# Kernel optimization log

Hardware: AMD Instinct MI355X
Metric: run time of the kernel (lower is better)

Reference implementation:

```python
import jax, jax.numpy as jnp
import numpy as np

B, S, H = 1, 4096, 768
NH, HD = 12, 64
THETA = 160000.0
WINDOW = 64  # local_attention=128 // 2
NEG = -1e9


def _rope_tables(seq_len, dim, theta):
    inv_freq = 1.0 / (theta ** (np.arange(0, dim, 2, dtype=np.float32) / dim))  # [dim/2]
    t = np.arange(seq_len, dtype=np.float32)
    freqs = np.outer(t, inv_freq)                      # [S, dim/2]
    emb = np.concatenate([freqs, freqs], axis=-1)      # [S, dim]
    return jnp.asarray(np.cos(emb)), jnp.asarray(np.sin(emb))


def _sliding_causal_mask(seq_len, window):
    i = np.arange(seq_len)[:, None]
    j = np.arange(seq_len)[None, :]
    allowed = (j <= i) & (i - j <= window)
    mask = np.where(allowed, 0.0, NEG).astype(np.float32)
    return jnp.asarray(mask)[None, None]  # [1,1,S,S]


def rotate_half(x):
    d = x.shape[-1] // 2
    return jnp.concatenate([-x[..., d:], x[..., :d]], axis=-1)


def setup_inputs() -> dict:
    key = jax.random.key(0)
    k1, k2, k3 = jax.random.split(key, 3)
    hidden_states = jax.random.normal(k1, (B, S, H), dtype=jnp.float32)
    w_qkv = jax.random.normal(k2, (3 * H, H), dtype=jnp.float32) * (H ** -0.5)
    w_o = jax.random.normal(k3, (H, H), dtype=jnp.float32) * (H ** -0.5)
    cos, sin = _rope_tables(S, HD, THETA)
    attention_mask = _sliding_causal_mask(S, WINDOW)
    return {"hidden_states": hidden_states, "w_qkv": w_qkv, "w_o": w_o,
            "cos": cos, "sin": sin, "attention_mask": attention_mask}


def reference(hidden_states, w_qkv, w_o, cos, sin, attention_mask):
    b, s, h = hidden_states.shape
    # QKV projection (no bias; attention_bias=False)
    qkv = jnp.einsum('bsh,oh->bso', hidden_states, w_qkv)        # [B,S,3H]
    qkv = qkv.reshape(b, s, 3, NH, HD)
    q = jnp.transpose(qkv[:, :, 0], (0, 2, 1, 3))                # [B,NH,S,HD]
    k = jnp.transpose(qkv[:, :, 1], (0, 2, 1, 3))
    v = jnp.transpose(qkv[:, :, 2], (0, 2, 1, 3))
    # RoPE
    c = cos[None, None]; sn = sin[None, None]                    # [1,1,S,HD]
    q = q * c + rotate_half(q) * sn
    k = k * c + rotate_half(k) * sn
    # eager attention: scaled QK^T + additive causal/sliding mask, fp32 softmax
    scaling = HD ** -0.5
    scores = jnp.einsum('bhqd,bhkd->bhqk', q, k) * scaling
    scores = scores + attention_mask[:, :, :, :s]
    attn = jax.nn.softmax(scores.astype(jnp.float32), axis=-1).astype(q.dtype)
    out = jnp.einsum('bhqk,bhkd->bhqd', attn, v)                 # [B,NH,S,HD]
    out = jnp.transpose(out, (0, 2, 1, 3)).reshape(b, s, h)
    return jnp.einsum('bsh,oh->bso', out, w_o)                   # Wo projection
```

## Files before the change

kernel.cpp:

```cpp
#include <hip/hip_runtime.h>

#define SLEN   4096
#define HDIM   768
#define NHEADS 12
#define HEADD  64
#define NQKV   2304
#define WIN    64

constexpr float SCALE = 0.125f;
constexpr float LOG2E = 1.4426950408889634f;

typedef short bf16x8 __attribute__((ext_vector_type(8)));
typedef float f32x4  __attribute__((ext_vector_type(4)));
typedef unsigned short u16;

#define MFMA(a, b, c) __builtin_amdgcn_mfma_f32_16x16x32_bf16((a), (b), (c), 0, 0, 0)

#define GLDS(gp, lp) __builtin_amdgcn_global_load_lds( \
    (const __attribute__((address_space(1))) unsigned*)(gp), \
    (__attribute__((address_space(3))) unsigned*)(lp), 16, 0, 0)

__device__ inline u16 f2bf(float x) {
    unsigned u = __float_as_uint(x);
    u += 0x7fff + ((u >> 16) & 1);
    return (u16)(u >> 16);
}
__device__ inline float bf2f(u16 b) { return __uint_as_float(((unsigned)b) << 16); }
__device__ inline unsigned packsplit(float x) {
    u16 h = f2bf(x);
    u16 l = f2bf(x - bf2f(h));
    return (unsigned)h | ((unsigned)l << 16);
}

__global__ __launch_bounds__(256) void split_planes(
    const float* __restrict__ hs, const float* __restrict__ wq, const float* __restrict__ wo,
    u16* __restrict__ hsH, u16* __restrict__ hsL,
    u16* __restrict__ wqH, u16* __restrict__ wqL,
    u16* __restrict__ woH, u16* __restrict__ woL)
{
    int qid = blockIdx.x * 256 + threadIdx.x;
    const float* src; u16 *dH, *dL; int r, k8;
    if (qid < 393216)      { src = hs; dH = hsH; dL = hsL; r = qid / 96; k8 = qid % 96; }
    else if (qid < 614400) { int q = qid - 393216; src = wq; dH = wqH; dL = wqL; r = q / 96; k8 = q % 96; }
    else                   { int q = qid - 614400; src = wo; dH = woH; dL = woL; r = q / 96; k8 = q % 96; }

    const float* p = src + (size_t)r * 768 + k8 * 8;
    float4 f0 = *(const float4*)p, f1 = *(const float4*)(p + 4);
    float fv[8] = {f0.x, f0.y, f0.z, f0.w, f1.x, f1.y, f1.z, f1.w};
    unsigned hh[4], ll[4];
#pragma unroll
    for (int i = 0; i < 4; ++i) {
        u16 h0 = f2bf(fv[2*i]),   h1 = f2bf(fv[2*i+1]);
        u16 l0 = f2bf(fv[2*i] - bf2f(h0)), l1 = f2bf(fv[2*i+1] - bf2f(h1));
        hh[i] = (unsigned)h0 | ((unsigned)h1 << 16);
        ll[i] = (unsigned)l0 | ((unsigned)l1 << 16);
    }
    size_t di = (size_t)r * 768 + (k8 >> 2) * 32 + (size_t)(((k8 & 3) ^ (r & 3))) * 8;
    *(uint4*)(dH + di) = uint4{hh[0], hh[1], hh[2], hh[3]};
    *(uint4*)(dL + di) = uint4{ll[0], ll[1], ll[2], ll[3]};
}

template <int MODE>
__global__ __launch_bounds__(256) void gemm_sp(
    const u16* __restrict__ Ah, const u16* __restrict__ Al,
    const u16* __restrict__ Bh, const u16* __restrict__ Bl,
    void* __restrict__ Cv, int M, int N, int K,
    const float* __restrict__ cosT, const float* __restrict__ sinT)
{
    __shared__ u16 sAh[4096], sAl[4096], sBh[4096], sBl[4096];

    const int tid = threadIdx.x;
    const int w = tid >> 6, lane = tid & 63;
    const int wr = w >> 1, wc = w & 1;
    const int l15 = lane & 15, l4 = lane >> 4;
    const int rowBase = blockIdx.y * 128, colBase = blockIdx.x * 128;
    const size_t strB = (size_t)K * 2;

    const char* Ahb = (const char*)Ah; const char* Alb = (const char*)Al;
    const char* Bhb = (const char*)Bh; const char* Blb = (const char*)Bl;

    f32x4 acc[4][4];
#pragma unroll
    for (int m = 0; m < 4; ++m)
#pragma unroll
        for (int n = 0; n < 4; ++n) acc[m][n] = f32x4{0.f, 0.f, 0.f, 0.f};

    const int nkt = K >> 5;
    for (int kt = 0; kt < nkt; ++kt) {
#pragma unroll
        for (int i = 0; i < 2; ++i) {
            int row  = i * 64 + w * 16 + (lane >> 2);
            int quad = lane & 3;
            size_t goA = (size_t)(rowBase + row) * strB + kt * 64 + quad * 16;
            size_t goB = (size_t)(colBase + row) * strB + kt * 64 + quad * 16;
            unsigned lo = i * 4096 + w * 1024;
            GLDS(Ahb + goA, (char*)sAh + lo);
            GLDS(Alb + goA, (char*)sAl + lo);
            GLDS(Bhb + goB, (char*)sBh + lo);
            GLDS(Blb + goB, (char*)sBl + lo);
        }
        __syncthreads();

        bf16x8 ah[4], al[4];
#pragma unroll
        for (int m = 0; m < 4; ++m) {
            int row = wr * 64 + m * 16 + l15;
            int byt = row * 64 + ((l4 * 16) ^ ((row & 3) << 4));
            ah[m] = *(const bf16x8*)((const char*)sAh + byt);
            al[m] = *(const bf16x8*)((const char*)sAl + byt);
        }
#pragma unroll
        for (int n = 0; n < 4; ++n) {
            int row = wc * 64 + n * 16 + l15;
            int byt = row * 64 + ((l4 * 16) ^ ((row & 3) << 4));
            bf16x8 bh = *(const bf16x8*)((const char*)sBh + byt);
            bf16x8 bl = *(const bf16x8*)((const char*)sBl + byt);
#pragma unroll
            for (int m = 0; m < 4; ++m) {
                acc[m][n] = MFMA(ah[m], bh, acc[m][n]);
                acc[m][n] = MFMA(ah[m], bl, acc[m][n]);
                acc[m][n] = MFMA(al[m], bh, acc[m][n]);
            }
        }
        __syncthreads();
    }

    if constexpr (MODE == 0) {
        float* C = (float*)Cv;
#pragma unroll
        for (int m = 0; m < 4; ++m)
#pragma unroll
            for (int n = 0; n < 4; ++n)
#pragma unroll
                for (int j = 0; j < 4; ++j) {
                    int row = rowBase + wr * 64 + m * 16 + l4 * 4 + j;
                    int col = colBase + wc * 64 + n * 16 + l15;
                    C[(size_t)row * N + col] = acc[m][n][j];
                }
    } else {
        unsigned* QKVp = (unsigned*)Cv;
        const int span = colBase + wc * 64;
        const int t = span / HDIM;
        const int hh = (span - t * HDIM) >> 6;
        unsigned* dstH = QKVp + (((size_t)t * NHEADS + hh) * SLEN) * HEADD;
#pragma unroll
        for (int m = 0; m < 4; ++m)
#pragma unroll
            for (int np = 0; np < 2; ++np)
#pragma unroll
                for (int j = 0; j < 4; ++j) {
                    int srow = rowBase + wr * 64 + m * 16 + l4 * 4 + j;
                    int dlo = np * 16 + l15;
                    float lo = acc[m][np][j];
                    float hi = acc[m][np + 2][j];
                    unsigned* dst = dstH + (size_t)srow * HEADD;
                    if (t < 2) {
                        float c = cosT[srow * HEADD + dlo];
                        float s = sinT[srow * HEADD + dlo];
                        float nlo = lo * c - hi * s;
                        float nhi = hi * c + lo * s;
                        dst[dlo]      = packsplit(nlo);
                        dst[dlo + 32] = packsplit(nhi);
                    } else {
                        dst[dlo]      = packsplit(lo);
                        dst[dlo + 32] = packsplit(hi);
                    }
                }
    }
}

__global__ __launch_bounds__(256) void attn_mfma(
    const unsigned* __restrict__ QKV, u16* __restrict__ OAh, u16* __restrict__ OAl)
{
    const int h  = blockIdx.x >> 6;
    const int qt = blockIdx.x & 63;
    const int qbase = qt << 6;
    const int kwin = qbase - 64;

    __shared__ u16 VTh[64 * 128], VTl[64 * 128];
    __shared__ u16 Ph_s[4][16 * 72], Pl_s[4][16 * 72];

    const unsigned* Qg = QKV + ((size_t)(0 * NHEADS + h) * SLEN) * HEADD;
    const unsigned* Kg = QKV + ((size_t)(1 * NHEADS + h) * SLEN) * HEADD;
    const unsigned* Vg = QKV + ((size_t)(2 * NHEADS + h) * SLEN) * HEADD;

    const int tid = threadIdx.x;
    const int w = tid >> 6, lane = tid & 63;
    const int l15 = lane & 15, l4 = lane >> 4;

#pragma unroll
    for (int i = 0; i < 4; ++i) {
        int idx = i * 256 + tid;
        int key = idx >> 3;
        int d8  = (idx & 7) * 8;
        int kg = kwin + key; if (kg < 0) kg = 0;
        const unsigned* vp = Vg + (size_t)kg * 64 + d8;
        uint4 p0 = *(const uint4*)vp, p1 = *(const uint4*)(vp + 4);
        unsigned vv[8] = {p0.x, p0.y, p0.z, p0.w, p1.x, p1.y, p1.z, p1.w};
#pragma unroll
        for (int j = 0; j < 8; ++j) {
            int d = d8 + j;
            int kk = key ^ ((d & 15) << 3);
            VTh[d * 128 + kk] = (u16)(vv[j] & 0xffff);
            VTl[d * 128 + kk] = (u16)(vv[j] >> 16);
        }
    }
    __syncthreads();

    const int qrow = qbase + w * 16 + l15;
    bf16x8 qh[2], ql[2];
#pragma unroll
    for (int ks = 0; ks < 2; ++ks) {
        const unsigned* qp = Qg + (size_t)qrow * 64 + ks * 32 + l4 * 8;
        uint4 a = *(const uint4*)qp, b = *(const uint4*)(qp + 4);
        union { unsigned u[4]; bf16x8 v; } H, L;
        H.u[0] = __builtin_amdgcn_perm(a.y, a.x, 0x05040100);
        H.u[1] = __builtin_amdgcn_perm(a.w, a.z, 0x05040100);
        H.u[2] = __builtin_amdgcn_perm(b.y, b.x, 0x05040100);
        H.u[3] = __builtin_amdgcn_perm(b.w, b.z, 0x05040100);
        L.u[0] = __builtin_amdgcn_perm(a.y, a.x, 0x07060302);
        L.u[1] = __builtin_amdgcn_perm(a.w, a.z, 0x07060302);
        L.u[2] = __builtin_amdgcn_perm(b.y, b.x, 0x07060302);
        L.u[3] = __builtin_amdgcn_perm(b.w, b.z, 0x07060302);
        qh[ks] = H.v; ql[ks] = L.v;
    }

    f32x4 st[8];
#pragma unroll
    for (int t = 0; t < 8; ++t) st[t] = f32x4{0.f, 0.f, 0.f, 0.f};
#pragma unroll
    for (int t = 0; t < 8; ++t) {
        int krow = kwin + 16 * t + l15; if (krow < 0) krow = 0;
#pragma unroll
        for (int ks = 0; ks < 2; ++ks) {
            const unsigned* kp = Kg + (size_t)krow * 64 + ks * 32 + l4 * 8;
            uint4 a = *(const uint4*)kp, b = *(const uint4*)(kp + 4);
            union { unsigned u[4]; bf16x8 v; } H, L;
            H.u[0] = __builtin_amdgcn_perm(a.y, a.x, 0x05040100);
            H.u[1] = __builtin_amdgcn_perm(a.w, a.z, 0x05040100);
            H.u[2] = __builtin_amdgcn_perm(b.y, b.x, 0x05040100);
            H.u[3] = __builtin_amdgcn_perm(b.w, b.z, 0x05040100);
            L.u[0] = __builtin_amdgcn_perm(a.y, a.x, 0x07060302);
            L.u[1] = __builtin_amdgcn_perm(a.w, a.z, 0x07060302);
            L.u[2] = __builtin_amdgcn_perm(b.y, b.x, 0x07060302);
            L.u[3] = __builtin_amdgcn_perm(b.w, b.z, 0x07060302);
            st[t] = MFMA(H.v, qh[ks], st[t]);
            st[t] = MFMA(H.v, ql[ks], st[t]);
            st[t] = MFMA(L.v, qh[ks], st[t]);
        }
    }

    const int qg = qrow;
    float mx = -1e30f;
#pragma unroll
    for (int t = 0; t < 8; ++t)
#pragma unroll
        for (int j = 0; j < 4; ++j) {
            int kg = kwin + 16 * t + 4 * l4 + j;
            float s = st[t][j] * SCALE;
            bool ok = (kg >= 0) && (kg <= qg) && (qg - kg <= WIN);
            s = ok ? s : -1e30f;
            st[t][j] = s;
            mx = fmaxf(mx, s);
        }
    mx = fmaxf(mx, __shfl_xor(mx, 16));
    mx = fmaxf(mx, __shfl_xor(mx, 32));
    float lsum = 0.f;
#pragma unroll
    for (int t = 0; t < 8; ++t)
#pragma unroll
        for (int j = 0; j < 4; ++j) {
            float p = exp2f((st[t][j] - mx) * LOG2E);
            st[t][j] = p;
            lsum += p;
        }
    lsum += __shfl_xor(lsum, 16);
    lsum += __shfl_xor(lsum, 32);

    f32x4 o[4];
#pragma unroll
    for (int dt = 0; dt < 4; ++dt) o[dt] = f32x4{0.f, 0.f, 0.f, 0.f};

#pragma unroll
    for (int half = 0; half < 2; ++half) {
#pragma unroll
        for (int tt = 0; tt < 4; ++tt) {
            int t = half * 4 + tt;
            u16 phv[4], plv[4];
#pragma unroll
            for (int j = 0; j < 4; ++j) {
                float p = st[t][j];
                phv[j] = f2bf(p);
                plv[j] = f2bf(p - bf2f(phv[j]));
            }
            int pidx = l15 * 72 + tt * 16 + l4 * 4;
            *(uint2*)&Ph_s[w][pidx] = uint2{(unsigned)phv[0] | ((unsigned)phv[1] << 16),
                                            (unsigned)phv[2] | ((unsigned)phv[3] << 16)};
            *(uint2*)&Pl_s[w][pidx] = uint2{(unsigned)plv[0] | ((unsigned)plv[1] << 16),
                                            (unsigned)plv[2] | ((unsigned)plv[3] << 16)};
        }
#pragma unroll
        for (int kss = 0; kss < 2; ++kss) {
            int koff = kss * 32 + l4 * 8;
            bf16x8 pbh = *(const bf16x8*)&Ph_s[w][l15 * 72 + koff];
            bf16x8 pbl = *(const bf16x8*)&Pl_s[w][l15 * 72 + koff];
            int K0 = half * 64 + kss * 32 + l4 * 8;
            int kk = K0 ^ (l15 << 3);
#pragma unroll
            for (int dt = 0; dt < 4; ++dt) {
                int d = dt * 16 + l15;
                bf16x8 vh = *(const bf16x8*)&VTh[d * 128 + kk];
                bf16x8 vl = *(const bf16x8*)&VTl[d * 128 + kk];
                o[dt] = MFMA(vh, pbh, o[dt]);
                o[dt] = MFMA(vh, pbl, o[dt]);
                o[dt] = MFMA(vl, pbh, o[dt]);
            }
        }
    }

    float inv = 1.0f / lsum;
    const int srow = qrow;
#pragma unroll
    for (int dt = 0; dt < 4; ++dt) {
        u16 hv[4], lv[4];
#pragma unroll
        for (int j = 0; j < 4; ++j) {
            float v = o[dt][j] * inv;
            hv[j] = f2bf(v);
            lv[j] = f2bf(v - bf2f(hv[j]));
        }
        int col0 = h * 64 + dt * 16 + l4 * 4;
        size_t di = (size_t)srow * 768 + (col0 >> 5) * 32
                  + (size_t)((((col0 >> 3) & 3) ^ (srow & 3))) * 8 + (col0 & 7);
        *(uint2*)(OAh + di) = uint2{(unsigned)hv[0] | ((unsigned)hv[1] << 16),
                                    (unsigned)hv[2] | ((unsigned)hv[3] << 16)};
        *(uint2*)(OAl + di) = uint2{(unsigned)lv[0] | ((unsigned)lv[1] << 16),
                                    (unsigned)lv[2] | ((unsigned)lv[3] << 16)};
    }
}

extern "C" void kernel_launch(void* const* d_in, const int* in_sizes, int n_in,
                              void* d_out, int out_size, void* d_ws, size_t ws_size,
                              hipStream_t stream)
{
    const float* hs   = (const float*)d_in[0];
    const float* wqkv = (const float*)d_in[1];
    const float* wo   = (const float*)d_in[2];
    const float* cosT = (const float*)d_in[3];
    const float* sinT = (const float*)d_in[4];
    float* out = (float*)d_out;

    char* p = (char*)d_ws;
    unsigned* qkvP = (unsigned*)p;      p += (size_t)3 * NHEADS * SLEN * HEADD * 4;
    u16* hsH = (u16*)p;                 p += (size_t)SLEN * HDIM * 2;
    u16* hsL = (u16*)p;                 p += (size_t)SLEN * HDIM * 2;
    u16* wqH = (u16*)p;                 p += (size_t)NQKV * HDIM * 2;
    u16* wqL = (u16*)p;                 p += (size_t)NQKV * HDIM * 2;
    u16* woH = (u16*)p;                 p += (size_t)HDIM * HDIM * 2;
    u16* woL = (u16*)p;                 p += (size_t)HDIM * HDIM * 2;
    u16* oAh = hsH;
    u16* oAl = hsL;

    split_planes<<<2688, 256, 0, stream>>>(hs, wqkv, wo, hsH, hsL, wqH, wqL, woH, woL);

    dim3 g1(NQKV / 128, SLEN / 128);
    gemm_sp<1><<<g1, 256, 0, stream>>>(hsH, hsL, wqH, wqL, qkvP, SLEN, NQKV, HDIM, cosT, sinT);

    attn_mfma<<<NHEADS * (SLEN / 64), 256, 0, stream>>>(qkvP, oAh, oAl);

    dim3 g2(HDIM / 128, SLEN / 128);
    gemm_sp<0><<<g2, 256, 0, stream>>>(oAh, oAl, woH, woL, out, SLEN, HDIM, HDIM, nullptr, nullptr);
}
```

Before: 248.9 us.

## Double-buffer LDS in split-bf16 GEMM, swizzle block order, smaller M tile for Wo

The split-precision GEMM now double-buffers its LDS tiles, issuing the global-to-LDS loads for the next K step before computing the current one, and drops one barrier per iteration. Blocks are launched on a 1D grid and remapped in a stride-8 interleaved order, intended to spread neighbouring tiles across XCDs. The output projection uses a 64-row M tile so it launches 384 blocks instead of 192 and fills more CUs. The cost is doubled LDS use, which may lower occupancy, and the prefetch into the other buffer depends on the single barrier per iteration for correctness.

```diff
diff --git a/kernel.cpp b/kernel.cpp
--- a/kernel.cpp
+++ b/kernel.cpp
@@ -60,80 +60,98 @@
     *(uint4*)(dL + di) = uint4{ll[0], ll[1], ll[2], ll[3]};
 }
 
-template <int MODE>
+template <int BM, int MODE>
 __global__ __launch_bounds__(256) void gemm_sp(
     const u16* __restrict__ Ah, const u16* __restrict__ Al,
     const u16* __restrict__ Bh, const u16* __restrict__ Bl,
-    void* __restrict__ Cv, int M, int N, int K,
-    const float* __restrict__ cosT, const float* __restrict__ sinT)
+    void* __restrict__ Cv, int N, int K,
+    const float* __restrict__ cosT, const float* __restrict__ sinT, int NBX)
 {
-    __shared__ u16 sAh[4096], sAl[4096], sBh[4096], sBl[4096];
+    constexpr int ASZ = BM * 32;
+    constexpr int MF  = BM / 32;
+    __shared__ u16 sAh[2][ASZ], sAl[2][ASZ], sBh[2][4096], sBl[2][4096];
 
     const int tid = threadIdx.x;
     const int w = tid >> 6, lane = tid & 63;
     const int wr = w >> 1, wc = w & 1;
     const int l15 = lane & 15, l4 = lane >> 4;
-    const int rowBase = blockIdx.y * 128, colBase = blockIdx.x * 128;
+    const int quad = lane & 3, rl = lane >> 2;
+
+    const int cpx = gridDim.x >> 3;
+    const int bsw = (blockIdx.x & 7) * cpx + (blockIdx.x >> 3);
+    const int bx = bsw % NBX, by = bsw / NBX;
+    const int rowBase = by * BM, colBase = bx * 128;
+
     const size_t strB = (size_t)K * 2;
-
     const char* Ahb = (const char*)Ah; const char* Alb = (const char*)Al;
     const char* Bhb = (const char*)Bh; const char* Blb = (const char*)Bl;
 
-    f32x4 acc[4][4];
-#pragma unroll
-    for (int m = 0; m < 4; ++m)
+    f32x4 acc[MF][4];
+#pragma unroll
+    for (int m = 0; m < MF; ++m)
 #pragma unroll
         for (int n = 0; n < 4; ++n) acc[m][n] = f32x4{0.f, 0.f, 0.f, 0.f};
 
+    auto stage = [&](int bi, int kt) {
+        size_t kb = (size_t)kt * 64 + quad * 16;
+#pragma unroll
+        for (int i = 0; i < BM / 64; ++i) {
+            int row = i * 64 + w * 16 + rl;
+            size_t go = (size_t)(rowBase + row) * strB + kb;
+            unsigned lo = i * 4096 + w * 1024;
+            GLDS(Ahb + go, (char*)(&sAh[bi][0]) + lo);
+            GLDS(Alb + go, (char*)(&sAl[bi][0]) + lo);
+        }
+#pragma unroll
+        for (int i = 0; i < 2; ++i) {
+            int row = i * 64 + w * 16 + rl;
+            size_t go = (size_t)(colBase + row) * strB + kb;
+            unsigned lo = i * 4096 + w * 1024;
+            GLDS(Bhb + go, (char*)(&sBh[bi][0]) + lo);
+            GLDS(Blb + go, (char*)(&sBl[bi][0]) + lo);
+        }
+    };
+
     const int nkt = K >> 5;
+    stage(0, 0);
+    int cur = 0;
     for (int kt = 0; kt < nkt; ++kt) {
-#pragma unroll
-        for (int i = 0; i < 2; ++i) {
-            int row  = i * 64 + w * 16 + (lane >> 2);
-            int quad = lane & 3;
-            size_t goA = (size_t)(rowBase + row) * strB + kt * 64 + quad * 16;
-            size_t goB = (size_t)(colBase + row) * strB + kt * 64 + quad * 16;
-            unsigned lo = i * 4096 + w * 1024;
-            GLDS(Ahb + goA, (char*)sAh + lo);
-            GLDS(Alb + goA, (char*)sAl + lo);
-            GLDS(Bhb + goB, (char*)sBh + lo);
-            GLDS(Blb + goB, (char*)sBl + lo);
-        }
         __syncthreads();
-
-        bf16x8 ah[4], al[4];
-#pragma unroll
-        for (int m = 0; m < 4; ++m) {
-            int row = wr * 64 + m * 16 + l15;
+        if (kt + 1 < nkt) stage(cur ^ 1, kt + 1);
+
+        bf16x8 ah[MF], al[MF];
+#pragma unroll
+        for (int m = 0; m < MF; ++m) {
+            int row = wr * (MF * 16) + m * 16 + l15;
             int byt = row * 64 + ((l4 * 16) ^ ((row & 3) << 4));
-            ah[m] = *(const bf16x8*)((const char*)sAh + byt);
-            al[m] = *(const bf16x8*)((const char*)sAl + byt);
+            ah[m] = *(const bf16x8*)((const char*)(&sAh[cur][0]) + byt);
+            al[m] = *(const bf16x8*)((const char*)(&sAl[cur][0]) + byt);
         }
 #pragma unroll
         for (int n = 0; n < 4; ++n) {
             int row = wc * 64 + n * 16 + l15;
             int byt = row * 64 + ((l4 * 16) ^ ((row & 3) << 4));
-            bf16x8 bh = *(const bf16x8*)((const char*)sBh + byt);
-            bf16x8 bl = *(const bf16x8*)((const char*)sBl + byt);
-#pragma unroll
-            for (int m = 0; m < 4; ++m) {
+            bf16x8 bh = *(const bf16x8*)((const char*)(&sBh[cur][0]) + byt);
+            bf16x8 bl = *(const bf16x8*)((const char*)(&sBl[cur][0]) + byt);
+#pragma unroll
+            for (int m = 0; m < MF; ++m) {
                 acc[m][n] = MFMA(ah[m], bh, acc[m][n]);
                 acc[m][n] = MFMA(ah[m], bl, acc[m][n]);
                 acc[m][n] = MFMA(al[m], bh, acc[m][n]);
             }
         }
-        __syncthreads();
+        cur ^= 1;
     }
 
     if constexpr (MODE == 0) {
         float* C = (float*)Cv;
 #pragma unroll
-        for (int m = 0; m < 4; ++m)
+        for (int m = 0; m < MF; ++m)
 #pragma unroll
             for (int n = 0; n < 4; ++n)
 #pragma unroll
                 for (int j = 0; j < 4; ++j) {
-                    int row = rowBase + wr * 64 + m * 16 + l4 * 4 + j;
+                    int row = rowBase + wr * (MF * 16) + m * 16 + l4 * 4 + j;
                     int col = colBase + wc * 64 + n * 16 + l15;
                     C[(size_t)row * N + col] = acc[m][n][j];
                 }
@@ -144,12 +162,12 @@
         const int hh = (span - t * HDIM) >> 6;
         unsigned* dstH = QKVp + (((size_t)t * NHEADS + hh) * SLEN) * HEADD;
 #pragma unroll
-        for (int m = 0; m < 4; ++m)
+        for (int m = 0; m < MF; ++m)
 #pragma unroll
             for (int np = 0; np < 2; ++np)
 #pragma unroll
                 for (int j = 0; j < 4; ++j) {
-                    int srow = rowBase + wr * 64 + m * 16 + l4 * 4 + j;
+                    int srow = rowBase + wr * (MF * 16) + m * 16 + l4 * 4 + j;
                     int dlo = np * 16 + l15;
                     float lo = acc[m][np][j];
                     float hi = acc[m][np + 2][j];
@@ -363,11 +381,11 @@
 
     split_planes<<<2688, 256, 0, stream>>>(hs, wqkv, wo, hsH, hsL, wqH, wqL, woH, woL);
 
-    dim3 g1(NQKV / 128, SLEN / 128);
-    gemm_sp<1><<<g1, 256, 0, stream>>>(hsH, hsL, wqH, wqL, qkvP, SLEN, NQKV, HDIM, cosT, sinT);
+    gemm_sp<128, 1><<<576, 256, 0, stream>>>(hsH, hsL, wqH, wqL, qkvP,
+                                             NQKV, HDIM, cosT, sinT, 18);
 
     attn_mfma<<<NHEADS * (SLEN / 64), 256, 0, stream>>>(qkvP, oAh, oAl);
 
-    dim3 g2(HDIM / 128, SLEN / 128);
-    gemm_sp<0><<<g2, 256, 0, stream>>>(oAh, oAl, woH, woL, out, SLEN, HDIM, HDIM, nullptr, nullptr);
-}
+    gemm_sp<64, 0><<<384, 256, 0, stream>>>(oAh, oAl, woH, woL, out,
+                                            HDIM, HDIM, nullptr, nullptr, 6);
+}
```

New measurement: 233.0 us. 1.07x faster.
